# Performance work log

Measured on AMD Instinct MI355X. Metric: run time of the kernel, lower is better.

The kernel has to match this reference:

```python
import jax, jax.numpy as jnp
import numpy as np

N_NODES = 100000
N_EDGES = 1600000
IN_CH = 64
HID = 128
OUT_CH = 2
N_GRAPHS = 512
LN_EPS = 1e-5


def setup_inputs() -> dict:
    key = jax.random.key(0)
    ks = jax.random.split(key, 16)
    x = jax.random.normal(ks[0], (N_NODES, IN_CH), dtype=jnp.float32)
    edge_index = jax.random.randint(ks[1], (2, N_EDGES), 0, N_NODES, dtype=jnp.int64)
    batch = jnp.sort(jax.random.randint(ks[2], (N_NODES,), 0, N_GRAPHS, dtype=jnp.int64))

    def lin(k, fan_in, fan_out):
        bound = 1.0 / np.sqrt(fan_in)
        return jax.random.uniform(k, (fan_in, fan_out), jnp.float32, -bound, bound)

    inp = {"x": x, "edge_index": edge_index, "batch": batch}
    # SAGEConv 0: in->hid; SAGEConv 1,2: hid->hid
    inp["Wl0"] = lin(ks[3], IN_CH, HID); inp["bl0"] = jnp.zeros((HID,), jnp.float32)
    inp["Wr0"] = lin(ks[4], IN_CH, HID)
    inp["Wl1"] = lin(ks[5], HID, HID); inp["bl1"] = jnp.zeros((HID,), jnp.float32)
    inp["Wr1"] = lin(ks[6], HID, HID)
    inp["Wl2"] = lin(ks[7], HID, HID); inp["bl2"] = jnp.zeros((HID,), jnp.float32)
    inp["Wr2"] = lin(ks[8], HID, HID)
    # decode: LayerNorm(hid) + Linear(hid, out)
    inp["ln_g"] = jnp.ones((HID,), jnp.float32)
    inp["ln_b"] = jnp.zeros((HID,), jnp.float32)
    inp["Wd"] = lin(ks[9], HID, OUT_CH)
    inp["bd"] = jnp.zeros((OUT_CH,), jnp.float32)
    return inp


def _sage_conv(x, src, dst, Wl, bl, Wr):
    # mean aggregation of source features onto destination nodes
    s = jax.ops.segment_sum(x[src], dst, num_segments=N_NODES)  # [N, F]
    cnt = jax.ops.segment_sum(jnp.ones((src.shape[0],), x.dtype), dst, num_segments=N_NODES)
    agg = s / jnp.maximum(cnt, 1.0)[:, None]
    return agg @ Wl + bl + x @ Wr


def reference(x, edge_index, batch, Wl0, bl0, Wr0, Wl1, bl1, Wr1, Wl2, bl2, Wr2, ln_g, ln_b, Wd, bd):
    src, dst = edge_index[0], edge_index[1]
    h = jax.nn.relu(_sage_conv(x, src, dst, Wl0, bl0, Wr0))
    h = jax.nn.relu(_sage_conv(h, src, dst, Wl1, bl1, Wr1))
    h = jax.nn.relu(_sage_conv(h, src, dst, Wl2, bl2, Wr2))
    # global_add_pool
    g = jax.ops.segment_sum(h, batch, num_segments=N_GRAPHS)  # [G, HID]
    # decode: LayerNorm + Linear
    mu = jnp.mean(g, axis=-1, keepdims=True)
    var = jnp.mean(jnp.square(g - mu), axis=-1, keepdims=True)
    gn = (g - mu) * jax.lax.rsqrt(var + LN_EPS) * ln_g + ln_b
    return gn @ Wd + bd
```

## Files before the change

kernel.cpp:

```cpp
#include <hip/hip_runtime.h>

#define N_NODES  100000
#define N_EDGES  1600000
#define N_GRAPHS 512
#define LN_EPS   1e-5f

#define NB    256
#define NPB   391
#define BCAP  8192
#define PCHUNK 8192
#define PBLOCKS ((N_EDGES + PCHUNK - 1) / PCHUNK)

typedef unsigned short u16;
typedef unsigned int   u32;
typedef __attribute__((ext_vector_type(8))) short bf16x8;
typedef __attribute__((ext_vector_type(4))) float f32x4;

__device__ __forceinline__ float b2f(u16 v) {
    u32 u = ((u32)v) << 16;
    return __builtin_bit_cast(float, u);
}
__device__ __forceinline__ u16 f2b(float f) {
    u32 u = __builtin_bit_cast(u32, f);
    u32 r = (u + 0x7fffu + ((u >> 16) & 1u)) >> 16;
    return (u16)r;
}


__global__ __launch_bounds__(256)
void partition_edges(const int* __restrict__ src, const int* __restrict__ dst,
                     int* __restrict__ bcnt, uint2* __restrict__ bpool) {
    __shared__ int hist[NB];
    __shared__ int gbase[NB];
    __shared__ int cur[NB];
    int t = threadIdx.x;
    int e0 = blockIdx.x * PCHUNK;
    int e1 = e0 + PCHUNK; if (e1 > N_EDGES) e1 = N_EDGES;

    hist[t] = 0;
    __syncthreads();
    for (int e = e0 + t; e < e1; e += 256)
        atomicAdd(&hist[dst[e] / NPB], 1);
    __syncthreads();
    int h = hist[t];
    gbase[t] = (h > 0) ? atomicAdd(&bcnt[t], h) : 0;
    cur[t] = 0;
    __syncthreads();
    for (int e = e0 + t; e < e1; e += 256) {
        int d = dst[e], s = src[e];
        int b = d / NPB;
        int p = atomicAdd(&cur[b], 1);
        bpool[(size_t)b * BCAP + gbase[b] + p] = make_uint2((u32)d, (u32)s);
    }
}

__global__ void scan_buckets(const int* __restrict__ bcnt, int* __restrict__ bbase,
                             int* __restrict__ offsets) {
    __shared__ int sh[NB];
    int t = threadIdx.x;
    int v = bcnt[t];
    sh[t] = v; __syncthreads();
    for (int off = 1; off < NB; off <<= 1) {
        int add = (t >= off) ? sh[t - off] : 0;
        __syncthreads();
        sh[t] += add;
        __syncthreads();
    }
    bbase[t] = sh[t] - v;
    if (t == NB - 1) offsets[N_NODES] = sh[t];
}

__global__ __launch_bounds__(256)
void build_csr_bucket(const int* __restrict__ bcnt, const int* __restrict__ bbase,
                      const uint2* __restrict__ bpool,
                      int* __restrict__ offsets, int* __restrict__ csr) {
    __shared__ int sA[512];
    __shared__ int sB[512];
    __shared__ int csrL[BCAP];
    int b = blockIdx.x, t = threadIdx.x;
    int nlo = b * NPB;
    int NL = N_NODES - nlo; if (NL > NPB) NL = NPB;
    int count = bcnt[b], base = bbase[b];
    const uint2* pool = bpool + (size_t)b * BCAP;

    sA[t] = 0; sA[t + 256] = 0;
    __syncthreads();
    for (int i = t; i < count; i += 256)
        atomicAdd(&sA[(int)pool[i].x - nlo], 1);
    __syncthreads();
    int c0 = sA[t], c1 = sA[t + 256];

    int* a = sA; int* c = sB;
    for (int off = 1; off < 512; off <<= 1) {
        c[t]       = a[t]       + ((t >= off)       ? a[t - off]       : 0);
        c[t + 256] = a[t + 256] + ((t + 256 >= off) ? a[t + 256 - off] : 0);
        __syncthreads();
        int* tmp = a; a = c; c = tmp;
    }
    int ex0 = a[t] - c0, ex1 = a[t + 256] - c1;
    if (t < NL)       offsets[nlo + t]       = base + ex0;
    if (t + 256 < NL) offsets[nlo + t + 256] = base + ex1;
    c[t] = ex0; c[t + 256] = ex1;
    __syncthreads();
    for (int i = t; i < count; i += 256) {
        uint2 p = pool[i];
        int pos = atomicAdd(&c[(int)p.x - nlo], 1);
        csrL[pos] = (int)p.y;
    }
    __syncthreads();
    for (int i = t; i < count; i += 256)
        csr[base + i] = csrL[i];
}


__global__ __launch_bounds__(256)
void conv_f32_bf16(const float* __restrict__ in, u16* __restrict__ out, int n4) {
    int i = blockIdx.x * 256 + threadIdx.x;
    if (i < n4) {
        float4 v = ((const float4*)in)[i];
        u32 lo = (u32)f2b(v.x) | ((u32)f2b(v.y) << 16);
        u32 hi = (u32)f2b(v.z) | ((u32)f2b(v.w) << 16);
        ((uint2*)out)[i] = make_uint2(lo, hi);
    }
}

__global__ __launch_bounds__(256)
void conv_weights(const float* __restrict__ Wl, const float* __restrict__ Wr,
                  int K1, int KC, u16* __restrict__ Wt) {
    int idx = blockIdx.x * 256 + threadIdx.x;
    if (idx >= 128 * KC) return;
    int c = idx / KC, k = idx % KC;
    float v = (k < K1) ? Wl[k * 128 + c] : Wr[(k - K1) * 128 + c];
    Wt[idx] = f2b(v);
}


template<int F>
__global__ __launch_bounds__(256)
void aggregate_bf16(const u16* __restrict__ in, const int* __restrict__ offsets,
                    const int* __restrict__ csr, u16* __restrict__ out) {
    int grp = threadIdx.x >> 5;
    int sub = threadIdx.x & 31;
    int n = blockIdx.x * 8 + grp;
    int o0 = offsets[n], o1 = offsets[n + 1];
    int d = o1 - o0;
    float inv = 1.0f / (float)(d > 1 ? d : 1);

    if (F == 128) {
        const uint2* base = (const uint2*)in;
        float acc[4][4];
        #pragma unroll
        for (int j = 0; j < 4; j++)
            #pragma unroll
            for (int c = 0; c < 4; c++) acc[j][c] = 0.f;

        int o = o0;
        for (; o + 4 <= o1; o += 4) {
            int s0 = csr[o + 0], s1 = csr[o + 1], s2 = csr[o + 2], s3 = csr[o + 3];
            uint2 v0 = base[(size_t)s0 * 32 + sub];
            uint2 v1 = base[(size_t)s1 * 32 + sub];
            uint2 v2 = base[(size_t)s2 * 32 + sub];
            uint2 v3 = base[(size_t)s3 * 32 + sub];
            acc[0][0] += b2f((u16)(v0.x & 0xffffu)); acc[0][1] += b2f((u16)(v0.x >> 16));
            acc[0][2] += b2f((u16)(v0.y & 0xffffu)); acc[0][3] += b2f((u16)(v0.y >> 16));
            acc[1][0] += b2f((u16)(v1.x & 0xffffu)); acc[1][1] += b2f((u16)(v1.x >> 16));
            acc[1][2] += b2f((u16)(v1.y & 0xffffu)); acc[1][3] += b2f((u16)(v1.y >> 16));
            acc[2][0] += b2f((u16)(v2.x & 0xffffu)); acc[2][1] += b2f((u16)(v2.x >> 16));
            acc[2][2] += b2f((u16)(v2.y & 0xffffu)); acc[2][3] += b2f((u16)(v2.y >> 16));
            acc[3][0] += b2f((u16)(v3.x & 0xffffu)); acc[3][1] += b2f((u16)(v3.x >> 16));
            acc[3][2] += b2f((u16)(v3.y & 0xffffu)); acc[3][3] += b2f((u16)(v3.y >> 16));
        }
        for (; o < o1; o++) {
            int s = csr[o];
            uint2 v = base[(size_t)s * 32 + sub];
            acc[0][0] += b2f((u16)(v.x & 0xffffu)); acc[0][1] += b2f((u16)(v.x >> 16));
            acc[0][2] += b2f((u16)(v.y & 0xffffu)); acc[0][3] += b2f((u16)(v.y >> 16));
        }
        float r0 = ((acc[0][0] + acc[1][0]) + (acc[2][0] + acc[3][0])) * inv;
        float r1 = ((acc[0][1] + acc[1][1]) + (acc[2][1] + acc[3][1])) * inv;
        float r2 = ((acc[0][2] + acc[1][2]) + (acc[2][2] + acc[3][2])) * inv;
        float r3 = ((acc[0][3] + acc[1][3]) + (acc[2][3] + acc[3][3])) * inv;
        uint2 w;
        w.x = (u32)f2b(r0) | ((u32)f2b(r1) << 16);
        w.y = (u32)f2b(r2) | ((u32)f2b(r3) << 16);
        ((uint2*)out)[(size_t)n * 32 + sub] = w;
    } else {
        const u32* base = (const u32*)in;
        float acc[4][2];
        #pragma unroll
        for (int j = 0; j < 4; j++) { acc[j][0] = 0.f; acc[j][1] = 0.f; }

        int o = o0;
        for (; o + 4 <= o1; o += 4) {
            int s0 = csr[o + 0], s1 = csr[o + 1], s2 = csr[o + 2], s3 = csr[o + 3];
            u32 v0 = base[(size_t)s0 * 32 + sub];
            u32 v1 = base[(size_t)s1 * 32 + sub];
            u32 v2 = base[(size_t)s2 * 32 + sub];
            u32 v3 = base[(size_t)s3 * 32 + sub];
            acc[0][0] += b2f((u16)(v0 & 0xffffu)); acc[0][1] += b2f((u16)(v0 >> 16));
            acc[1][0] += b2f((u16)(v1 & 0xffffu)); acc[1][1] += b2f((u16)(v1 >> 16));
            acc[2][0] += b2f((u16)(v2 & 0xffffu)); acc[2][1] += b2f((u16)(v2 >> 16));
            acc[3][0] += b2f((u16)(v3 & 0xffffu)); acc[3][1] += b2f((u16)(v3 >> 16));
        }
        for (; o < o1; o++) {
            int s = csr[o];
            u32 v = base[(size_t)s * 32 + sub];
            acc[0][0] += b2f((u16)(v & 0xffffu)); acc[0][1] += b2f((u16)(v >> 16));
        }
        float r0 = ((acc[0][0] + acc[1][0]) + (acc[2][0] + acc[3][0])) * inv;
        float r1 = ((acc[0][1] + acc[1][1]) + (acc[2][1] + acc[3][1])) * inv;
        ((u32*)out)[(size_t)n * 32 + sub] = (u32)f2b(r0) | ((u32)f2b(r1) << 16);
    }
}


template<int KHALF>
__global__ __launch_bounds__(256)
void gemm_mfma(const u16* __restrict__ A1, const u16* __restrict__ A2,
               const u16* __restrict__ Wt, const float* __restrict__ bias,
               u16* __restrict__ out) {
    constexpr int KC  = 2 * KHALF;
    constexpr int NKS = KC / 32;

    int t = threadIdx.x;
    int lane = t & 63, w = t >> 6;
    int l15 = lane & 15, l4 = lane >> 4;
    int mbase = blockIdx.x * 64;

    bf16x8 bfr[2][NKS];
    #pragma unroll
    for (int ct = 0; ct < 2; ct++)
        #pragma unroll
        for (int ks = 0; ks < NKS; ks++) {
            int row = w * 32 + ct * 16 + l15;
            int kb  = ks * 32 + l4 * 8;
            bfr[ct][ks] = *reinterpret_cast<const bf16x8*>(Wt + row * KC + kb);
        }

    f32x4 acc[4][2];
    #pragma unroll
    for (int i = 0; i < 4; i++)
        #pragma unroll
        for (int j = 0; j < 2; j++)
            acc[i][j] = (f32x4){0.f, 0.f, 0.f, 0.f};

    const bf16x8 zfr = {0, 0, 0, 0, 0, 0, 0, 0};

    #pragma unroll
    for (int ks = 0; ks < NKS; ks++) {
        const u16* Ab = (ks < NKS / 2) ? A1 : A2;
        int kb = (ks < NKS / 2) ? (ks * 32 + l4 * 8) : ((ks - NKS / 2) * 32 + l4 * 8);
        bf16x8 afr[4];
        #pragma unroll
        for (int rt = 0; rt < 4; rt++) {
            int row = mbase + rt * 16 + l15;
            afr[rt] = (row < N_NODES)
                ? *reinterpret_cast<const bf16x8*>(Ab + (size_t)row * KHALF + kb)
                : zfr;
        }
        #pragma unroll
        for (int rt = 0; rt < 4; rt++)
            #pragma unroll
            for (int ct = 0; ct < 2; ct++)
                acc[rt][ct] = __builtin_amdgcn_mfma_f32_16x16x32_bf16(
                    afr[rt], bfr[ct][ks], acc[rt][ct], 0, 0, 0);
    }

    #pragma unroll
    for (int ct = 0; ct < 2; ct++) {
        int col = w * 32 + ct * 16 + l15;
        float bv = bias[col];
        #pragma unroll
        for (int rt = 0; rt < 4; rt++) {
            #pragma unroll
            for (int j = 0; j < 4; j++) {
                int row = mbase + rt * 16 + l4 * 4 + j;
                if (row < N_NODES) {
                    float v = fmaxf(acc[rt][ct][j] + bv, 0.f);
                    out[(size_t)row * 128 + col] = f2b(v);
                }
            }
        }
    }
}


__global__ __launch_bounds__(128)
void pool_ln_decode(const u16* __restrict__ h, const int* __restrict__ batch,
                    const float* __restrict__ ln_g, const float* __restrict__ ln_b,
                    const float* __restrict__ Wd, const float* __restrict__ bd,
                    float* __restrict__ out) {
    __shared__ float red[128];
    __shared__ int bounds[2];
    int g = blockIdx.x, c = threadIdx.x;
    if (c < 2) {
        int target = g + c;
        int lo = 0, hi = N_NODES;
        while (lo < hi) {
            int mid = (lo + hi) >> 1;
            if (batch[mid] < target) lo = mid + 1; else hi = mid;
        }
        bounds[c] = lo;
    }
    __syncthreads();
    int start = bounds[0], end = bounds[1];

    float s = 0.f;
    for (int r = start; r < end; r++) s += b2f(h[(size_t)r * 128 + c]);

    red[c] = s; __syncthreads();
    for (int off = 64; off > 0; off >>= 1) {
        if (c < off) red[c] += red[c + off];
        __syncthreads();
    }
    float mu = red[0] * (1.0f / 128.f);
    __syncthreads();

    float d = s - mu;
    red[c] = d * d; __syncthreads();
    for (int off = 64; off > 0; off >>= 1) {
        if (c < off) red[c] += red[c + off];
        __syncthreads();
    }
    float var = red[0] * (1.0f / 128.f);
    __syncthreads();

    float gn = d * rsqrtf(var + LN_EPS) * ln_g[c] + ln_b[c];

    red[c] = gn * Wd[c * 2 + 0]; __syncthreads();
    for (int off = 64; off > 0; off >>= 1) {
        if (c < off) red[c] += red[c + off];
        __syncthreads();
    }
    float o0 = red[0];
    __syncthreads();

    red[c] = gn * Wd[c * 2 + 1]; __syncthreads();
    for (int off = 64; off > 0; off >>= 1) {
        if (c < off) red[c] += red[c + off];
        __syncthreads();
    }
    if (c == 0) {
        out[g * 2 + 0] = o0 + bd[0];
        out[g * 2 + 1] = red[0] + bd[1];
    }
}


extern "C" void kernel_launch(void* const* d_in, const int* in_sizes, int n_in,
                              void* d_out, int out_size, void* d_ws, size_t ws_size,
                              hipStream_t stream) {
    (void)in_sizes; (void)n_in; (void)out_size; (void)ws_size;

    const float* x     = (const float*)d_in[0];
    const int*   ei    = (const int*)d_in[1];
    const int*   batch = (const int*)d_in[2];
    const float* Wl0 = (const float*)d_in[3];
    const float* bl0 = (const float*)d_in[4];
    const float* Wr0 = (const float*)d_in[5];
    const float* Wl1 = (const float*)d_in[6];
    const float* bl1 = (const float*)d_in[7];
    const float* Wr1 = (const float*)d_in[8];
    const float* Wl2 = (const float*)d_in[9];
    const float* bl2 = (const float*)d_in[10];
    const float* Wr2 = (const float*)d_in[11];
    const float* ln_g = (const float*)d_in[12];
    const float* ln_b = (const float*)d_in[13];
    const float* Wd  = (const float*)d_in[14];
    const float* bd  = (const float*)d_in[15];
    float* out = (float*)d_out;

    const int* src = ei;
    const int* dst = ei + N_EDGES;

    char* ws = (char*)d_ws;
    int*   csr     = (int*)(ws + 0);
    int*   offsets = (int*)(ws + 6400000);
    int*   bcnt    = (int*)(ws + 6800128);
    int*   bbase   = (int*)(ws + 6801152);
    uint2* bpool   = (uint2*)(ws + 6802176);
    u16*   x16     = (u16*)(ws + 23579392);
    u16*   aggbuf  = (u16*)(ws + 36379392);
    u16*   bufB    = (u16*)(ws + 61979392);
    u16*   bufC    = (u16*)(ws + 87579392);
    u16*   Wt0     = (u16*)(ws + 113179392);
    u16*   Wt1     = (u16*)(ws + 113212160);
    u16*   Wt2     = (u16*)(ws + 113277696);

    hipMemsetAsync(bcnt, 0, NB * sizeof(int), stream);

    partition_edges<<<PBLOCKS, 256, 0, stream>>>(src, dst, bcnt, bpool);
    scan_buckets<<<1, 256, 0, stream>>>(bcnt, bbase, offsets);
    build_csr_bucket<<<NB, 256, 0, stream>>>(bcnt, bbase, bpool, offsets, csr);

    conv_f32_bf16<<<(N_NODES * 64 / 4 + 255) / 256, 256, 0, stream>>>(x, x16, N_NODES * 64 / 4);
    conv_weights<<<(128 * 128 + 255) / 256, 256, 0, stream>>>(Wl0, Wr0, 64, 128, Wt0);
    conv_weights<<<(128 * 256 + 255) / 256, 256, 0, stream>>>(Wl1, Wr1, 128, 256, Wt1);
    conv_weights<<<(128 * 256 + 255) / 256, 256, 0, stream>>>(Wl2, Wr2, 128, 256, Wt2);

    const int aggGrid  = N_NODES / 8;
    const int gemmGrid = (N_NODES + 63) / 64;

    aggregate_bf16<64><<<aggGrid, 256, 0, stream>>>(x16, offsets, csr, aggbuf);
    gemm_mfma<64><<<gemmGrid, 256, 0, stream>>>(aggbuf, x16, Wt0, bl0, bufB);
    aggregate_bf16<128><<<aggGrid, 256, 0, stream>>>(bufB, offsets, csr, aggbuf);
    gemm_mfma<128><<<gemmGrid, 256, 0, stream>>>(aggbuf, bufB, Wt1, bl1, bufC);
    aggregate_bf16<128><<<aggGrid, 256, 0, stream>>>(bufC, offsets, csr, aggbuf);
    gemm_mfma<128><<<gemmGrid, 256, 0, stream>>>(aggbuf, bufC, Wt2, bl2, bufB);

    pool_ln_decode<<<N_GRAPHS, 128, 0, stream>>>(bufB, batch, ln_g, ln_b, Wd, bd, out);
}
```

Before: 424.4 us.

## Split graph pooling into chunked atomic partial sums plus wave-level LN decode

Replaces the one-block-per-graph pooling kernel, which walked about 195 rows serially per graph, with a kernel that gives each block a 64-node chunk and flushes per-graph running sums into a float buffer with atomics. A second small kernel then does the LayerNorm and the linear decode with wave shuffles instead of shared-memory tree reductions. The aim is more parallel blocks and shorter serial chains, at the cost of an extra memset, an extra launch and float atomics whose summation order varies from run to run.

```diff
diff --git a/kernel.cpp b/kernel.cpp
--- a/kernel.cpp
+++ b/kernel.cpp
@@ -10,6 +10,8 @@
 #define BCAP  8192
 #define PCHUNK 8192
 #define PBLOCKS ((N_EDGES + PCHUNK - 1) / PCHUNK)
+#define POOL_CHUNK 64
+#define POOL_BLOCKS ((N_NODES + POOL_CHUNK - 1) / POOL_CHUNK)
 
 typedef unsigned short u16;
 typedef unsigned int   u32;
@@ -286,63 +288,53 @@
 
 
 __global__ __launch_bounds__(128)
-void pool_ln_decode(const u16* __restrict__ h, const int* __restrict__ batch,
-                    const float* __restrict__ ln_g, const float* __restrict__ ln_b,
-                    const float* __restrict__ Wd, const float* __restrict__ bd,
-                    float* __restrict__ out) {
-    __shared__ float red[128];
-    __shared__ int bounds[2];
-    int g = blockIdx.x, c = threadIdx.x;
-    if (c < 2) {
-        int target = g + c;
-        int lo = 0, hi = N_NODES;
-        while (lo < hi) {
-            int mid = (lo + hi) >> 1;
-            if (batch[mid] < target) lo = mid + 1; else hi = mid;
-        }
-        bounds[c] = lo;
-    }
-    __syncthreads();
-    int start = bounds[0], end = bounds[1];
-
-    float s = 0.f;
-    for (int r = start; r < end; r++) s += b2f(h[(size_t)r * 128 + c]);
-
-    red[c] = s; __syncthreads();
-    for (int off = 64; off > 0; off >>= 1) {
-        if (c < off) red[c] += red[c + off];
-        __syncthreads();
-    }
-    float mu = red[0] * (1.0f / 128.f);
-    __syncthreads();
-
-    float d = s - mu;
-    red[c] = d * d; __syncthreads();
-    for (int off = 64; off > 0; off >>= 1) {
-        if (c < off) red[c] += red[c + off];
-        __syncthreads();
-    }
-    float var = red[0] * (1.0f / 128.f);
-    __syncthreads();
-
-    float gn = d * rsqrtf(var + LN_EPS) * ln_g[c] + ln_b[c];
-
-    red[c] = gn * Wd[c * 2 + 0]; __syncthreads();
-    for (int off = 64; off > 0; off >>= 1) {
-        if (c < off) red[c] += red[c + off];
-        __syncthreads();
-    }
-    float o0 = red[0];
-    __syncthreads();
-
-    red[c] = gn * Wd[c * 2 + 1]; __syncthreads();
-    for (int off = 64; off > 0; off >>= 1) {
-        if (c < off) red[c] += red[c + off];
-        __syncthreads();
-    }
-    if (c == 0) {
+void pool_partial(const u16* __restrict__ h, const int* __restrict__ batch,
+                  float* __restrict__ gpool) {
+    int c = threadIdx.x;
+    int n0 = blockIdx.x * POOL_CHUNK;
+    int n1 = n0 + POOL_CHUNK; if (n1 > N_NODES) n1 = N_NODES;
+    float run = 0.f;
+    int curg = -1;
+    for (int r = n0; r < n1; r++) {
+        int gid = batch[r];
+        if (gid != curg) {
+            if (curg >= 0) atomicAdd(&gpool[curg * 128 + c], run);
+            run = 0.f; curg = gid;
+        }
+        run += b2f(h[(size_t)r * 128 + c]);
+    }
+    if (curg >= 0) atomicAdd(&gpool[curg * 128 + c], run);
+}
+
+__global__ __launch_bounds__(64)
+void ln_decode(const float* __restrict__ gpool,
+               const float* __restrict__ ln_g, const float* __restrict__ ln_b,
+               const float* __restrict__ Wd, const float* __restrict__ bd,
+               float* __restrict__ out) {
+    int g = blockIdx.x, lane = threadIdx.x;
+    float v0 = gpool[g * 128 + lane];
+    float v1 = gpool[g * 128 + 64 + lane];
+    float s = v0 + v1;
+    #pragma unroll
+    for (int off = 32; off > 0; off >>= 1) s += __shfl_xor(s, off, 64);
+    float mu = s * (1.0f / 128.f);
+    float d0 = v0 - mu, d1 = v1 - mu;
+    float q = d0 * d0 + d1 * d1;
+    #pragma unroll
+    for (int off = 32; off > 0; off >>= 1) q += __shfl_xor(q, off, 64);
+    float rs = rsqrtf(q * (1.0f / 128.f) + LN_EPS);
+    float gn0 = d0 * rs * ln_g[lane]      + ln_b[lane];
+    float gn1 = d1 * rs * ln_g[64 + lane] + ln_b[64 + lane];
+    float o0 = gn0 * Wd[lane * 2 + 0] + gn1 * Wd[(64 + lane) * 2 + 0];
+    float o1 = gn0 * Wd[lane * 2 + 1] + gn1 * Wd[(64 + lane) * 2 + 1];
+    #pragma unroll
+    for (int off = 32; off > 0; off >>= 1) {
+        o0 += __shfl_xor(o0, off, 64);
+        o1 += __shfl_xor(o1, off, 64);
+    }
+    if (lane == 0) {
         out[g * 2 + 0] = o0 + bd[0];
-        out[g * 2 + 1] = red[0] + bd[1];
+        out[g * 2 + 1] = o1 + bd[1];
     }
 }
 
@@ -386,8 +378,10 @@
     u16*   Wt0     = (u16*)(ws + 113179392);
     u16*   Wt1     = (u16*)(ws + 113212160);
     u16*   Wt2     = (u16*)(ws + 113277696);
+    float* gpool   = (float*)(ws + 113343232);
 
     hipMemsetAsync(bcnt, 0, NB * sizeof(int), stream);
+    hipMemsetAsync(gpool, 0, N_GRAPHS * 128 * sizeof(float), stream);
 
     partition_edges<<<PBLOCKS, 256, 0, stream>>>(src, dst, bcnt, bpool);
     scan_buckets<<<1, 256, 0, stream>>>(bcnt, bbase, offsets);
@@ -408,5 +402,6 @@
     aggregate_bf16<128><<<aggGrid, 256, 0, stream>>>(bufC, offsets, csr, aggbuf);
     gemm_mfma<128><<<gemmGrid, 256, 0, stream>>>(aggbuf, bufC, Wt2, bl2, bufB);
 
-    pool_ln_decode<<<N_GRAPHS, 128, 0, stream>>>(bufB, batch, ln_g, ln_b, Wd, bd, out);
-}
+    pool_partial<<<POOL_BLOCKS, 128, 0, stream>>>(bufB, batch, gpool);
+    ln_decode<<<N_GRAPHS, 64, 0, stream>>>(gpool, ln_g, ln_b, Wd, bd, out);
+}
```

Measured after the change: 375.4 us. 11.5% less time.
